# Performance work log

Measured on AMD Instinct MI355X. Metric: run time of the kernel, lower is better.

Reference implementation:

```python
import jax, jax.numpy as jnp
import numpy as np


def _conv1x1(x, W, b):
    # 1x1 conv == per-pixel channel matmul: x [B,C,H,W], W [O,C], b [O]
    return jnp.einsum('bchw,oc->bohw', x, W) + b[None, :, None, None]


def setup_inputs() -> dict:
    key = jax.random.key(0)
    ks = jax.random.split(key, 9)
    B, C, H, W = 16, 512, 32, 32
    s = 1.0 / np.sqrt(C)
    inp = {
        'x': jax.random.normal(ks[0], (B, C, H, W), dtype=jnp.float32),
        'Wq': jax.random.normal(ks[1], (C, C), dtype=jnp.float32) * s,
        'bq': jax.random.normal(ks[2], (C,), dtype=jnp.float32) * 0.01,
        'Wk': jax.random.normal(ks[3], (C, C), dtype=jnp.float32) * s,
        'bk': jax.random.normal(ks[4], (C,), dtype=jnp.float32) * 0.01,
        'Wv': jax.random.normal(ks[5], (C, C), dtype=jnp.float32) * s,
        'bv': jax.random.normal(ks[6], (C,), dtype=jnp.float32) * 0.01,
        'Wo': jax.random.normal(ks[7], (C, C), dtype=jnp.float32) * s,
        'bo': jax.random.normal(ks[8], (C,), dtype=jnp.float32) * 0.01,
    }
    return inp


def reference(x, Wq, bq, Wk, bk, Wv, bv, Wo, bo):
    B, C, H, W = x.shape
    q = _conv1x1(x, Wq, bq)
    k = _conv1x1(x, Wk, bk)
    v = _conv1x1(x, Wv, bv)
    hw = H * W
    qf = q.reshape(B, C, hw)  # [B,C,HW]
    kf = k.reshape(B, C, hw)
    vf = v.reshape(B, C, hw)
    # scores[b,i,j] = sum_c q[b,c,i] * k[b,c,j], scaled by c^-0.5
    scores = jnp.einsum('bci,bcj->bij', qf, kf) * (C ** -0.5)
    attn = jax.nn.softmax(scores, axis=2)  # softmax over keys j
    # out[b,c,i] = sum_j v[b,c,j] * attn[b,i,j]
    out = jnp.einsum('bcj,bij->bci', vf, attn).reshape(B, C, H, W)
    out = _conv1x1(out, Wo, bo)
    return x + out
```

## Files before the change

### kernel.cpp

```cpp
#include <hip/hip_runtime.h>
#include <hip/hip_bf16.h>
#include <math.h>


typedef __bf16 bf16x8 __attribute__((ext_vector_type(8)));
typedef float  f32x4  __attribute__((ext_vector_type(4)));

__device__ __forceinline__ unsigned short f2bf(float f) {
    unsigned u = __float_as_uint(f);
    u += 0x7fff + ((u >> 16) & 1);
    return (unsigned short)(u >> 16);
}

__device__ __forceinline__ void gload_lds16(const void* g, void* l) {
    __builtin_amdgcn_global_load_lds(
        (const __attribute__((address_space(1))) void*)g,
        (__attribute__((address_space(3))) void*)l, 16, 0, 0);
}

struct GemmP {
    const unsigned short* A;
    const unsigned short* B;
    void* C;
    const float* bias;
    const float* resid;
    int M, N, K, ldA, ldB;
    long sA, sB, sC, sR;
    int ln_nn, ln_pb;
    float scale;
};

template<bool OUT_F32, int BIAS_MODE, bool RESID, int EXPM>
__device__ __forceinline__ void gemm_body(const GemmP p, int L,
                                          unsigned short* Als,
                                          unsigned short* Bls)
{
    const int xcd = L & 7;
    const int idx = L >> 3;
    const int bz  = xcd * 2 + (idx >> p.ln_pb);
    const int w   = idx & ((1 << p.ln_pb) - 1);
    const int m0  = (w >> p.ln_nn) << 7;
    const int n0  = (w & ((1 << p.ln_nn) - 1)) << 7;

    const unsigned short* A = p.A + bz * p.sA;
    const unsigned short* B = p.B + bz * p.sB;

    const int tid  = threadIdx.x;
    const int lane = tid & 63;
    const int wave = tid >> 6;
    const int wm   = wave >> 1;
    const int wn   = wave & 1;

    const int ar = lane >> 2;
    const int ak = (lane & 3) * 8;

    const unsigned short* agp = A + (long)(m0 + wave * 16 + ar) * p.ldA + ak;
    const unsigned short* bgp = B + (long)(n0 + wave * 16 + ar) * p.ldB + ak;
    const long aj = 64L * p.ldA;
    const long bj = 64L * p.ldB;

    const int fr = lane & 15;
    const int fq = lane >> 4;

    f32x4 acc[4][4] = {};
    f32x4 acc1[4] = {};
    bf16x8 ones;
    if constexpr (EXPM == 2) {
        #pragma unroll
        for (int i = 0; i < 8; ++i) ones[i] = (__bf16)1.0f;
    }

    const int nsteps = p.K >> 5;

    auto STAGE = [&](int sel) {
        unsigned short* a0 = Als + sel * 4096;
        unsigned short* b0 = Bls + sel * 4096;
        gload_lds16(agp,      a0 + wave * 512);
        gload_lds16(agp + aj, a0 + (wave + 4) * 512);
        gload_lds16(bgp,      b0 + wave * 512);
        gload_lds16(bgp + bj, b0 + (wave + 4) * 512);
        agp += 32; bgp += 32;
    };

    auto COMPUTE = [&](int sel) {
        const unsigned short* Ap = Als + sel * 4096;
        const unsigned short* Bp = Bls + sel * 4096;
        bf16x8 af[4], bfr[4];
        #pragma unroll
        for (int mt = 0; mt < 4; ++mt)
            af[mt] = *(const bf16x8*)&Ap[(wm * 64 + mt * 16 + fr) * 32 + fq * 8];
        #pragma unroll
        for (int nt = 0; nt < 4; ++nt)
            bfr[nt] = *(const bf16x8*)&Bp[(wn * 64 + nt * 16 + fr) * 32 + fq * 8];
        if constexpr (EXPM == 2) {
            #pragma unroll
            for (int mt = 0; mt < 4; ++mt)
                acc1[mt] = __builtin_amdgcn_mfma_f32_16x16x32_bf16(
                    af[mt], ones, acc1[mt], 0, 0, 0);
        }
        #pragma unroll
        for (int mt = 0; mt < 4; ++mt)
            #pragma unroll
            for (int nt = 0; nt < 4; ++nt)
                acc[mt][nt] = __builtin_amdgcn_mfma_f32_16x16x32_bf16(
                    af[mt], bfr[nt], acc[mt][nt], 0, 0, 0);
    };

    STAGE(0);
    STAGE(1);

    int bc = 0, bn = 1, bs = 2;
    for (int t = 0; t < nsteps - 1; ++t) {
        __builtin_amdgcn_sched_barrier(0);
        asm volatile("s_waitcnt vmcnt(4)" ::: "memory");
        __builtin_amdgcn_s_barrier();
        asm volatile("" ::: "memory");
        __builtin_amdgcn_sched_barrier(0);
        if (t + 2 < nsteps) STAGE(bs);
        COMPUTE(bc);
        const int tmp = bc; bc = bn; bn = bs; bs = tmp;
    }
    __builtin_amdgcn_sched_barrier(0);
    asm volatile("s_waitcnt vmcnt(0)" ::: "memory");
    __builtin_amdgcn_s_barrier();
    asm volatile("" ::: "memory");
    __builtin_amdgcn_sched_barrier(0);
    COMPUTE(bc);

    float* Cf = (float*)p.C + bz * p.sC;
    unsigned short* Ch = (unsigned short*)p.C + bz * p.sC;
    const float* resid = RESID ? (p.resid + bz * p.sR) : nullptr;
    const int N = p.N;

    if constexpr (EXPM == 1) {
        #pragma unroll
        for (int mt = 0; mt < 4; ++mt)
            #pragma unroll
            for (int r = 0; r < 4; ++r) {
                const int row = m0 + wm * 64 + mt * 16 + fq * 4 + r;
                #pragma unroll
                for (int nt = 0; nt < 4; ++nt) {
                    const int col = n0 + wn * 64 + nt * 16 + fr;
                    Ch[(long)row * N + col] = f2bf(__expf(acc[mt][nt][r] * p.scale));
                }
            }
    } else {
        #pragma unroll
        for (int mt = 0; mt < 4; ++mt) {
            float linv[4];
            if constexpr (EXPM == 2) {
                #pragma unroll
                for (int r = 0; r < 4; ++r)
                    linv[r] = 1.0f / acc1[mt][r];
            }
            #pragma unroll
            for (int nt = 0; nt < 4; ++nt) {
                const int col = n0 + wn * 64 + nt * 16 + fr;
                const float bn2 = (BIAS_MODE == 2) ? p.bias[col] : 0.0f;
                #pragma unroll
                for (int r = 0; r < 4; ++r) {
                    const int row = m0 + wm * 64 + mt * 16 + fq * 4 + r;
                    float val = acc[mt][nt][r] + bn2;
                    if (BIAS_MODE == 1) val += p.bias[row];
                    if constexpr (EXPM == 2) val *= linv[r];
                    const long o = (long)row * N + col;
                    if (RESID) val += resid[o];
                    if (OUT_F32) Cf[o] = val;
                    else         Ch[o] = f2bf(val);
                }
            }
        }
    }
}

template<bool OUT_F32, int BIAS_MODE, bool RESID, int EXPM>
__global__ __launch_bounds__(256, 3) void gemm_bt_mfma(GemmP p)
{
    __shared__ unsigned short Als[3 * 4096];
    __shared__ unsigned short Bls[3 * 4096];
    gemm_body<OUT_F32, BIAS_MODE, RESID, EXPM>(p, blockIdx.x, Als, Bls);
}

__global__ __launch_bounds__(256, 3) void gemm_qkv_fused(GemmP pqk, GemmP pv, int split)
{
    __shared__ unsigned short Als[3 * 4096];
    __shared__ unsigned short Bls[3 * 4096];
    if ((int)blockIdx.x < split)
        gemm_body<false, 2, false, 0>(pqk, blockIdx.x, Als, Bls);
    else
        gemm_body<false, 1, false, 0>(pv, blockIdx.x - split, Als, Bls);
}

__global__ __launch_bounds__(256) void prep_all(
    const float* __restrict__ x, unsigned short* __restrict__ xT,
    const float* __restrict__ Wq, const float* __restrict__ Wk,
    const float* __restrict__ Wv, const float* __restrict__ Wo,
    const float* __restrict__ bq, const float* __restrict__ bk,
    unsigned short* __restrict__ Wb, float* __restrict__ biasqk)
{
    const int b = blockIdx.x;
    const int t = threadIdx.x;
    if (b < 8192) {
        __shared__ float tl[32][33];
        const int batch = b >> 9;
        const int rem = b & 511;
        const int p0 = (rem & 31) * 32;
        const int c0 = (rem >> 5) * 32;
        const float* xb = x + (long)batch * 524288;
        unsigned short* xTb = xT + (long)batch * 524288;
        const int tx = t & 31;
        const int ty = t >> 5;
        #pragma unroll
        for (int i = 0; i < 4; ++i)
            tl[ty + 8 * i][tx] = xb[(long)(c0 + ty + 8 * i) * 1024 + p0 + tx];
        __syncthreads();
        #pragma unroll
        for (int i = 0; i < 4; ++i)
            xTb[(long)(p0 + ty + 8 * i) * 512 + c0 + tx] = f2bf(tl[tx][ty + 8 * i]);
    } else if (b < 9216) {
        const int wb = b - 8192;
        const float* srcs[4] = {Wq, Wk, Wv, Wo};
        const float* s = srcs[wb >> 8];
        unsigned short* d = Wb + (long)(wb >> 8) * 262144;
        const int i = ((wb & 255) * 256 + t) * 4;
        const float4 f = *(const float4*)(s + i);
        ushort4 h;
        h.x = f2bf(f.x); h.y = f2bf(f.y); h.z = f2bf(f.z); h.w = f2bf(f.w);
        *(ushort4*)(d + i) = h;
    } else {
        biasqk[t]       = bq[t];
        biasqk[256 + t] = bq[256 + t];
        biasqk[512 + t] = bk[t];
        biasqk[768 + t] = bk[256 + t];
    }
}

extern "C" void kernel_launch(void* const* d_in, const int* in_sizes, int n_in,
                              void* d_out, int out_size, void* d_ws, size_t ws_size,
                              hipStream_t stream)
{
    const float* x  = (const float*)d_in[0];
    const float* Wq = (const float*)d_in[1];
    const float* bq = (const float*)d_in[2];
    const float* Wk = (const float*)d_in[3];
    const float* bk = (const float*)d_in[4];
    const float* Wv = (const float*)d_in[5];
    const float* bv = (const float*)d_in[6];
    const float* Wo = (const float*)d_in[7];
    const float* bo = (const float*)d_in[8];
    float* out = (float*)d_out;

    const int Bn = 16, C = 512, HW = 1024;
    const long CHW = (long)C * HW;
    const long SHW = (long)HW * HW;

    unsigned short* xT   = (unsigned short*)d_ws;
    unsigned short* qkT  = xT + Bn * CHW;
    unsigned short* vB   = qkT + Bn * SHW;
    unsigned short* expS = vB + Bn * CHW;
    unsigned short* Wb   = expS + Bn * SHW;
    float* biasqk = (float*)(Wb + 4 * 262144);
    unsigned short* OT = xT;

    unsigned short* Wvb = Wb + 2 * 262144;
    unsigned short* Wob = Wb + 3 * 262144;

    const dim3 blk(256);
    const float scale = 0.044194173824159216f;

    prep_all<<<dim3(9217), blk, 0, stream>>>(x, xT, Wq, Wk, Wv, Wo, bq, bk,
                                             Wb, biasqk);

    GemmP pqk = { xT, Wb, qkT, biasqk, nullptr,
                  HW, 2 * C, C, C, C, CHW, 0, SHW, 0, 3, 6, 0.0f };
    GemmP pv  = { Wvb, xT, vB, bv, nullptr,
                  C, HW, C, C, C, 0, CHW, CHW, 0, 3, 5, 0.0f };
    gemm_qkv_fused<<<dim3(1536), blk, 0, stream>>>(pqk, pv, 1024);

    GemmP ps  = { qkT, qkT + C, expS, nullptr, nullptr,
                  HW, HW, C, 2 * C, 2 * C, SHW, SHW, SHW, 0, 3, 6, scale };
    gemm_bt_mfma<false, 0, false, 1><<<dim3(1024), blk, 0, stream>>>(ps);

    GemmP po  = { expS, vB, OT, nullptr, nullptr,
                  HW, C, HW, HW, HW, SHW, CHW, CHW, 0, 2, 5, 0.0f };
    gemm_bt_mfma<false, 0, false, 2><<<dim3(512), blk, 0, stream>>>(po);

    GemmP pout = { Wob, OT, out, bo, x,
                   C, HW, C, C, C, 0, CHW, CHW, CHW, 3, 5, 0.0f };
    gemm_bt_mfma<true, 1, true, 0><<<dim3(512), blk, 0, stream>>>(pout);
}
```

Baseline: 219.7 us.

## Swizzle GEMM LDS tiles and widen x transpose to 64x64 bf16 tiles

The GEMM LDS staging now XOR-swizzles the k-chunk position by row, on both the global-to-LDS write and the fragment reads, to cut LDS bank conflicts in the MFMA operand loads. The x transpose in the prep kernel moves to 64x64 tiles with float4 loads, converts to bf16 before staging, and uses an XOR-swizzled bf16 shared tile. This means fewer blocks and wider global transactions. The transpose's read-back still does scalar 16-bit LDS reads, and the swizzle has to match exactly across writer and reader.

```diff
diff --git a/kernel.cpp b/kernel.cpp
--- a/kernel.cpp
+++ b/kernel.cpp
@@ -52,7 +52,7 @@
     const int wn   = wave & 1;
 
     const int ar = lane >> 2;
-    const int ak = (lane & 3) * 8;
+    const int ak = ((lane & 3) ^ ((ar >> 1) & 3)) * 8;
 
     const unsigned short* agp = A + (long)(m0 + wave * 16 + ar) * p.ldA + ak;
     const unsigned short* bgp = B + (long)(n0 + wave * 16 + ar) * p.ldB + ak;
@@ -61,6 +61,7 @@
 
     const int fr = lane & 15;
     const int fq = lane >> 4;
+    const int kphys = (fq ^ ((fr >> 1) & 3)) * 8;
 
     f32x4 acc[4][4] = {};
     f32x4 acc1[4] = {};
@@ -88,10 +89,10 @@
         bf16x8 af[4], bfr[4];
         #pragma unroll
         for (int mt = 0; mt < 4; ++mt)
-            af[mt] = *(const bf16x8*)&Ap[(wm * 64 + mt * 16 + fr) * 32 + fq * 8];
+            af[mt] = *(const bf16x8*)&Ap[(wm * 64 + mt * 16 + fr) * 32 + kphys];
         #pragma unroll
         for (int nt = 0; nt < 4; ++nt)
-            bfr[nt] = *(const bf16x8*)&Bp[(wn * 64 + nt * 16 + fr) * 32 + fq * 8];
+            bfr[nt] = *(const bf16x8*)&Bp[(wn * 64 + nt * 16 + fr) * 32 + kphys];
         if constexpr (EXPM == 2) {
             #pragma unroll
             for (int mt = 0; mt < 4; ++mt)
@@ -200,25 +201,46 @@
 {
     const int b = blockIdx.x;
     const int t = threadIdx.x;
-    if (b < 8192) {
-        __shared__ float tl[32][33];
-        const int batch = b >> 9;
-        const int rem = b & 511;
-        const int p0 = (rem & 31) * 32;
-        const int c0 = (rem >> 5) * 32;
+    if (b < 2048) {
+        __shared__ unsigned short tlb[64 * 64];
+        const int batch = b >> 7;
+        const int rem = b & 127;
+        const int c0 = (rem >> 4) * 64;
+        const int p0 = (rem & 15) * 64;
         const float* xb = x + (long)batch * 524288;
         unsigned short* xTb = xT + (long)batch * 524288;
-        const int tx = t & 31;
-        const int ty = t >> 5;
-        #pragma unroll
-        for (int i = 0; i < 4; ++i)
-            tl[ty + 8 * i][tx] = xb[(long)(c0 + ty + 8 * i) * 1024 + p0 + tx];
+        const int lx = t & 15;
+        const int ly = t >> 4;
+        #pragma unroll
+        for (int i = 0; i < 4; ++i) {
+            const int c = ly + 16 * i;
+            const float4 f = *(const float4*)&xb[(long)(c0 + c) * 1024 + p0 + lx * 4];
+            ushort4 h;
+            h.x = f2bf(f.x); h.y = f2bf(f.y); h.z = f2bf(f.z); h.w = f2bf(f.w);
+            const int colp = (lx * 4) ^ (((c >> 3) & 7) << 3);
+            *(ushort4*)&tlb[c * 64 + colp] = h;
+        }
         __syncthreads();
-        #pragma unroll
-        for (int i = 0; i < 4; ++i)
-            xTb[(long)(p0 + ty + 8 * i) * 512 + c0 + tx] = f2bf(tl[tx][ty + 8 * i]);
-    } else if (b < 9216) {
-        const int wb = b - 8192;
+        const int sx = t & 7;
+        const int sy = t >> 3;
+        #pragma unroll
+        for (int i = 0; i < 2; ++i) {
+            const int r = sy + 32 * i;
+            ushort4 lo, hi;
+            lo.x = tlb[(sx * 8 + 0) * 64 + (r ^ (sx << 3))];
+            lo.y = tlb[(sx * 8 + 1) * 64 + (r ^ (sx << 3))];
+            lo.z = tlb[(sx * 8 + 2) * 64 + (r ^ (sx << 3))];
+            lo.w = tlb[(sx * 8 + 3) * 64 + (r ^ (sx << 3))];
+            hi.x = tlb[(sx * 8 + 4) * 64 + (r ^ (sx << 3))];
+            hi.y = tlb[(sx * 8 + 5) * 64 + (r ^ (sx << 3))];
+            hi.z = tlb[(sx * 8 + 6) * 64 + (r ^ (sx << 3))];
+            hi.w = tlb[(sx * 8 + 7) * 64 + (r ^ (sx << 3))];
+            unsigned short* o = &xTb[(long)(p0 + r) * 512 + c0 + sx * 8];
+            *(ushort4*)o = lo;
+            *(ushort4*)(o + 4) = hi;
+        }
+    } else if (b < 3072) {
+        const int wb = b - 2048;
         const float* srcs[4] = {Wq, Wk, Wv, Wo};
         const float* s = srcs[wb >> 8];
         unsigned short* d = Wb + (long)(wb >> 8) * 262144;
@@ -268,7 +290,7 @@
     const dim3 blk(256);
     const float scale = 0.044194173824159216f;
 
-    prep_all<<<dim3(9217), blk, 0, stream>>>(x, xT, Wq, Wk, Wv, Wo, bq, bk,
+    prep_all<<<dim3(3073), blk, 0, stream>>>(x, xT, Wq, Wk, Wv, Wo, bq, bk,
                                              Wb, biasqk);
 
     GemmP pqk = { xT, Wb, qkT, biasqk, nullptr,
```

New measurement: 216.6 us. About the same (-1.4%).
